# Kernel optimization log

Measured on AMD Instinct MI355X. Metric: run time of the kernel, lower is better.

The kernel has to match this reference:

```python
import jax, jax.numpy as jnp
import numpy as np
import math

B, C, H, W = 16, 512, 32, 32
NUM_HEADS = 8
EPS = 1e-5

def setup_inputs() -> dict:
    key = jax.random.key(0)
    ks = jax.random.split(key, 4)
    x = jax.random.normal(ks[0], (B, C, H, W), dtype=jnp.float32)
    emb = jax.random.normal(ks[1], (B, C), dtype=jnp.float32)
    w_qkv = jax.random.normal(ks[2], (3 * C, C), dtype=jnp.float32) * (1.0 / math.sqrt(C))
    b_qkv = jnp.zeros((3 * C,), dtype=jnp.float32)
    w_proj = jax.random.normal(ks[3], (C, C), dtype=jnp.float32) * (1.0 / math.sqrt(C))
    b_proj = jnp.zeros((C,), dtype=jnp.float32)
    return {"x": x, "emb": emb, "w_qkv": w_qkv, "b_qkv": b_qkv, "w_proj": w_proj, "b_proj": b_proj}


def reference(x, emb, w_qkv, b_qkv, w_proj, b_proj):
    b, c = x.shape[0], x.shape[1]
    spatial = x.shape[2:]
    xf = x.reshape(b, c, -1)                      # [b, c, T]
    # LayerNorm over channel dim (dim=1), no affine
    mu = jnp.mean(xf, axis=1, keepdims=True)
    var = jnp.var(xf, axis=1, keepdims=True)
    xn = (xf - mu) / jnp.sqrt(var + EPS)
    # 1x1 conv = channel GEMM: [3c,c] x [b,c,T] -> [b,3c,T]
    qkv = jnp.einsum('oc,bct->bot', w_qkv, xn) + b_qkv[None, :, None]
    T = qkv.shape[-1]
    qkv = qkv.reshape(b * NUM_HEADS, -1, T)       # [b*h, 3*hd, T]
    ch = qkv.shape[1] // 3
    q, k, v = jnp.split(qkv, 3, axis=1)
    scale = 1.0 / math.sqrt(math.sqrt(ch))
    w = jnp.einsum('bct,bcs->bts', q * scale, k * scale)  # [b*h, T, T]
    w = jax.nn.softmax(w.astype(jnp.float32), axis=-1).astype(qkv.dtype)
    h = jnp.einsum('bts,bcs->bct', w, v)          # [b*h, hd, T]
    h = h.reshape(b, -1, T)                        # [b, c, T]
    h = jnp.einsum('oc,bct->bot', w_proj, h) + b_proj[None, :, None]
    return (xf + h).reshape(b, c, *spatial)
```

## Files before the change

kernel.cpp:

```cpp
#include <hip/hip_runtime.h>


#define TSZ 1024
#define CCH 512
#define NBATCH 16

typedef __attribute__((ext_vector_type(8))) short short8;
typedef __attribute__((ext_vector_type(4))) float f32x4;
typedef __attribute__((ext_vector_type(4))) int i32x4;
typedef __attribute__((ext_vector_type(4))) unsigned u32x4;
typedef __attribute__((ext_vector_type(2))) unsigned u32x2;

__device__ inline short f2bf(float f) {
  unsigned u = __builtin_bit_cast(unsigned, f);
  u += 0x7fff + ((u >> 16) & 1);
  return (short)(u >> 16);
}

__device__ inline void gl16(const void* g, void* l) {
  __builtin_amdgcn_global_load_lds((const __attribute__((address_space(1))) void*)g,
                                   (__attribute__((address_space(3))) void*)l,
                                   16, 0, 0);
}

__global__ __launch_bounds__(256) void k_cvt(const float* __restrict__ wq,
                                             const float* __restrict__ wp,
                                             short* __restrict__ wqb,
                                             short* __restrict__ wpb) {
  int i = blockIdx.x * 256 + threadIdx.x;
  const int nq = 1536 * 512;
  if (i < nq) wqb[i] = f2bf(wq[i]);
  int j = i - nq;
  if (j >= 0 && j < 512 * 512) wpb[j] = f2bf(wp[j]);
}

__global__ __launch_bounds__(256) void k_ln(const float* __restrict__ x,
                                            short* __restrict__ xnT) {
  const int b = blockIdx.x;
  const int t0 = blockIdx.y * 64;
  const int tid = threadIdx.x;
  const int tt = tid & 63, cg = tid >> 6;

  __shared__ float red[2][4][64];
  __shared__ float mu_s[64], rs_s[64];
  __shared__ float xt[64][65];

  const float* xb = x + (long)b * CCH * TSZ;

  float s = 0.f, s2 = 0.f;
  for (int c = cg * 128; c < cg * 128 + 128; ++c) {
    float v = xb[(long)c * TSZ + t0 + tt];
    s += v; s2 += v * v;
  }
  red[0][cg][tt] = s; red[1][cg][tt] = s2;
  __syncthreads();
  if (tid < 64) {
    float ss = red[0][0][tid] + red[0][1][tid] + red[0][2][tid] + red[0][3][tid];
    float qq = red[1][0][tid] + red[1][1][tid] + red[1][2][tid] + red[1][3][tid];
    float mu = ss * (1.f / 512.f);
    float var = qq * (1.f / 512.f) - mu * mu;
    mu_s[tid] = mu;
    rs_s[tid] = rsqrtf(var + 1e-5f);
  }
  __syncthreads();

  for (int c0 = 0; c0 < CCH; c0 += 64) {
    for (int i = tid; i < 64 * 64; i += 256) {
      int ci = i >> 6, t2 = i & 63;
      xt[ci][t2] = xb[(long)(c0 + ci) * TSZ + t0 + t2];
    }
    __syncthreads();
    for (int i = tid; i < 64 * 64; i += 256) {
      int cc = i & 63, t2 = i >> 6;
      float v = (xt[cc][t2] - mu_s[t2]) * rs_s[t2];
      xnT[((long)b * TSZ + t0 + t2) * CCH + c0 + cc] = f2bf(v);
    }
    __syncthreads();
  }
}

__device__ inline int qkmap(int n) {
  if (n < 512) return (n >> 6) * 192 + (n & 63);
  int j = n - 512;
  return (j >> 6) * 192 + 64 + (j & 63);
}
__device__ inline int vmap(int m) {
  return (m >> 6) * 192 + 128 + (m & 63);
}

template <int MODE>
__global__ __launch_bounds__(256) void k_gemm(const short* __restrict__ Ab,
                                              const short* __restrict__ Bb,
                                              void* __restrict__ outb,
                                              const float* __restrict__ bias,
                                              const float* __restrict__ resid) {
  const int b = blockIdx.z;
  const int m0 = blockIdx.x * 128, n0 = blockIdx.y * 128;
  const int tid = threadIdx.x;
  const int lane = tid & 63, wv = tid >> 6;
  const int wm = wv >> 1, wn = wv & 1;
  const int l15 = lane & 15, lg = lane >> 4;

  const short* A = Ab + (MODE == 0 ? (long)b * TSZ * CCH : 0);
  const short* Bm = Bb + (MODE == 0 ? 0 : (long)b * TSZ * CCH);

  __shared__ __attribute__((aligned(16))) short sA[128 * 32];
  __shared__ __attribute__((aligned(16))) short sB[128 * 32];

  f32x4 acc[4][4];
#pragma unroll
  for (int i = 0; i < 4; ++i)
#pragma unroll
    for (int j = 0; j < 4; ++j) acc[i][j] = (f32x4){0.f, 0.f, 0.f, 0.f};

  long a_src[2], b_src[2];
#pragma unroll
  for (int q = 0; q < 2; ++q) {
    int idx = wv * 128 + q * 64 + lane;
    int row = idx >> 2, kc = (idx & 3) * 8;
    int am = m0 + row;
    int ar = (MODE == 1) ? vmap(am) : am;
    a_src[q] = (long)ar * CCH + kc;
    int bn = n0 + row;
    int br = (MODE == 0) ? qkmap(bn) : bn;
    b_src[q] = (long)br * CCH + kc;
  }

  for (int k0 = 0; k0 < CCH; k0 += 32) {
#pragma unroll
    for (int q = 0; q < 2; ++q) {
      gl16(A + a_src[q] + k0, sA + (wv * 128 + q * 64) * 8);
      gl16(Bm + b_src[q] + k0, sB + (wv * 128 + q * 64) * 8);
    }
    __syncthreads();
    short8 af[4], bfr[4];
#pragma unroll
    for (int i = 0; i < 4; ++i)
      af[i] = *(const short8*)(sA + ((wm * 64 + i * 16 + l15) * 32 + lg * 8));
#pragma unroll
    for (int j = 0; j < 4; ++j)
      bfr[j] = *(const short8*)(sB + ((wn * 64 + j * 16 + l15) * 32 + lg * 8));
#pragma unroll
    for (int i = 0; i < 4; ++i)
#pragma unroll
      for (int j = 0; j < 4; ++j)
        acc[i][j] = __builtin_amdgcn_mfma_f32_16x16x32_bf16(af[i], bfr[j], acc[i][j], 0, 0, 0);
    __syncthreads();
  }

#pragma unroll
  for (int i = 0; i < 4; ++i)
#pragma unroll
    for (int j = 0; j < 4; ++j)
#pragma unroll
      for (int r = 0; r < 4; ++r) {
        int mi = m0 + wm * 64 + i * 16 + lg * 4 + r;
        int ni = n0 + wn * 64 + j * 16 + l15;
        float val = acc[i][j][r];
        long o = (long)mi * TSZ + ni;
        if (MODE == 0) {
          val += bias[qkmap(ni)];
          if (ni < 512) val *= 0.18033688011112042f;
          ((short*)outb)[(long)b * TSZ * TSZ + o] = f2bf(val);
        } else if (MODE == 1) {
          val += bias[vmap(mi)];
          ((short*)outb)[(long)b * CCH * TSZ + o] = f2bf(val);
        } else {
          val += bias[mi] + resid[(long)b * CCH * TSZ + o];
          ((float*)outb)[(long)b * CCH * TSZ + o] = val;
        }
      }
}

__global__ __launch_bounds__(256, 4) void k_attn(const short* __restrict__ qk,
                                                 const short* __restrict__ vbuf,
                                                 short* __restrict__ hb) {
  const int wgid = blockIdx.y * gridDim.x + blockIdx.x;
  const int xcd = wgid & 7, kb = wgid >> 3;
  const int bh = xcd * 16 + (kb & 15);
  const int t0 = (kb >> 4) * 128;
  const int b = bh >> 3, h = bh & 7;
  const int tid = threadIdx.x;
  const int lane = tid & 63, w = tid >> 6;
  const int l15 = lane & 15, lg = lane >> 4;

  __shared__ __attribute__((aligned(16))) short kt[2][64 * 64];
  __shared__ __attribute__((aligned(16))) short vt[2][64 * 64];

  const short* qkb = qk + (long)b * TSZ * 1024;
  const short* vb = vbuf + (long)b * CCH * TSZ;

  short8 aq[2][2];
  {
    const short* qb = qkb + (long)(t0 + w * 32) * 1024 + h * 64;
#pragma unroll
    for (int jt = 0; jt < 2; ++jt)
#pragma unroll
      for (int kk = 0; kk < 2; ++kk)
        aq[jt][kk] = *(const short8*)(qb + (long)(jt * 16 + l15) * 1024 + kk * 32 + lg * 8);
  }

  f32x4 of[2][4];
  float lp[2] = {0.f, 0.f};
#pragma unroll
  for (int i = 0; i < 2; ++i)
#pragma unroll
    for (int nf = 0; nf < 4; ++nf) of[i][nf] = (f32x4){0.f, 0.f, 0.f, 0.f};

  int srow[2], scoff[2];
#pragma unroll
  for (int q = 0; q < 2; ++q) {
    int idx = w * 128 + q * 64 + lane;
    int row = idx >> 3;
    int byo = ((idx & 7) * 16) ^ ((row & 7) << 4);
    srow[q] = row;
    scoff[q] = byo >> 1;
  }

  long vsrc[2];
  int vdstA[2], vdstB[2];
#pragma unroll
  for (int q = 0; q < 2; ++q) {
    int idx = q * 256 + tid;
    int c = idx >> 3, s8 = (idx & 7) * 8;
    vsrc[q] = (long)(h * 64 + c) * TSZ + s8;
    int kk2 = s8 >> 5, h4 = (s8 >> 4) & 1, lgf0 = (s8 & 15) >> 2;
    int spA = kk2 * 32 + lgf0 * 8 + h4 * 4;
    vdstA[q] = ((c * 64 + spA) * 2) ^ ((c & 7) << 4);
    vdstB[q] = ((c * 64 + spA + 8) * 2) ^ ((c & 7) << 4);
  }

#define STAGE_K(buf, s0s)                                                      \
  {                                                                            \
    _Pragma("unroll") for (int q = 0; q < 2; ++q)                              \
      gl16(qkb + (long)((s0s) + srow[q]) * 1024 + 512 + h * 64 + scoff[q],     \
           kt[buf] + (w * 128 + q * 64) * 8);                                  \
  }

  u32x4 vreg0 = *(const u32x4*)(vb + vsrc[0]);
  u32x4 vreg1 = *(const u32x4*)(vb + vsrc[1]);
  STAGE_K(0, 0);
  *(u32x2*)((char*)vt[0] + vdstA[0]) = (u32x2){vreg0.x, vreg0.y};
  *(u32x2*)((char*)vt[0] + vdstB[0]) = (u32x2){vreg0.z, vreg0.w};
  *(u32x2*)((char*)vt[0] + vdstA[1]) = (u32x2){vreg1.x, vreg1.y};
  *(u32x2*)((char*)vt[0] + vdstB[1]) = (u32x2){vreg1.z, vreg1.w};
  __syncthreads();

  for (int s0 = 0; s0 < TSZ; s0 += 64) {
    const int cur = (s0 >> 6) & 1;
    const bool np = (s0 + 64 < TSZ);
    if (np) {
      vreg0 = *(const u32x4*)(vb + vsrc[0] + s0 + 64);
      vreg1 = *(const u32x4*)(vb + vsrc[1] + s0 + 64);
      STAGE_K(cur ^ 1, s0 + 64);
    }

    f32x4 sf[2][4];
#pragma unroll
    for (int jt = 0; jt < 2; ++jt)
#pragma unroll
      for (int ms = 0; ms < 4; ++ms) sf[jt][ms] = (f32x4){0.f, 0.f, 0.f, 0.f};
#pragma unroll
    for (int kk = 0; kk < 2; ++kk)
#pragma unroll
      for (int ms = 0; ms < 4; ++ms) {
        int srw = ms * 16 + l15;
        int byo = ((srw * 64 + kk * 32 + lg * 8) * 2) ^ ((srw & 7) << 4);
        short8 ka = *(const short8*)((const char*)kt[cur] + byo);
#pragma unroll
        for (int jt = 0; jt < 2; ++jt)
          sf[jt][ms] = __builtin_amdgcn_mfma_f32_16x16x32_bf16(ka, aq[jt][kk], sf[jt][ms], 0, 0, 0);
      }

    short8 apf[2][2];
#pragma unroll
    for (int jt = 0; jt < 2; ++jt) {
      float p[4][4];
#pragma unroll
      for (int ms = 0; ms < 4; ++ms)
#pragma unroll
        for (int r = 0; r < 4; ++r)
          p[ms][r] = exp2f(sf[jt][ms][r]);
#pragma unroll
      for (int ms = 0; ms < 4; ++ms)
        lp[jt] += (p[ms][0] + p[ms][1]) + (p[ms][2] + p[ms][3]);
      unsigned pk[4][2];
#pragma unroll
      for (int ms = 0; ms < 4; ++ms)
#pragma unroll
        for (int u = 0; u < 2; ++u)
          asm("v_cvt_pk_bf16_f32 %0, %1, %2" : "=v"(pk[ms][u])
              : "v"(p[ms][2 * u]), "v"(p[ms][2 * u + 1]));
#pragma unroll
      for (int kk = 0; kk < 2; ++kk) {
        i32x4 a32 = (i32x4){(int)pk[2 * kk][0], (int)pk[2 * kk][1],
                            (int)pk[2 * kk + 1][0], (int)pk[2 * kk + 1][1]};
        apf[jt][kk] = __builtin_bit_cast(short8, a32);
      }
    }

#pragma unroll
    for (int kk = 0; kk < 2; ++kk)
#pragma unroll
      for (int nf = 0; nf < 4; ++nf) {
        int cc = nf * 16 + l15;
        int byo = ((cc * 64 + kk * 32 + lg * 8) * 2) ^ ((cc & 7) << 4);
        short8 bv = *(const short8*)((const char*)vt[cur] + byo);
#pragma unroll
        for (int i = 0; i < 2; ++i)
          of[i][nf] = __builtin_amdgcn_mfma_f32_16x16x32_bf16(apf[i][kk], bv, of[i][nf], 0, 0, 0);
      }

    if (np) {
      *(u32x2*)((char*)vt[cur ^ 1] + vdstA[0]) = (u32x2){vreg0.x, vreg0.y};
      *(u32x2*)((char*)vt[cur ^ 1] + vdstB[0]) = (u32x2){vreg0.z, vreg0.w};
      *(u32x2*)((char*)vt[cur ^ 1] + vdstA[1]) = (u32x2){vreg1.x, vreg1.y};
      *(u32x2*)((char*)vt[cur ^ 1] + vdstB[1]) = (u32x2){vreg1.z, vreg1.w};
    }
    __syncthreads();
  }

  float linv[2][4];
#pragma unroll
  for (int i = 0; i < 2; ++i) {
    float ls = lp[i];
    ls += __shfl_xor(ls, 16);
    ls += __shfl_xor(ls, 32);
#pragma unroll
    for (int r = 0; r < 4; ++r)
      linv[i][r] = 1.0f / __shfl(ls, lg * 4 + r);
  }

#pragma unroll
  for (int i = 0; i < 2; ++i)
#pragma unroll
    for (int nf = 0; nf < 4; ++nf)
#pragma unroll
      for (int r = 0; r < 4; ++r) {
        int t = t0 + w * 32 + i * 16 + lg * 4 + r;
        int c = h * 64 + nf * 16 + l15;
        hb[((long)b * TSZ + t) * CCH + c] = f2bf(of[i][nf][r] * linv[i][r]);
      }
}

extern "C" void kernel_launch(void* const* d_in, const int* in_sizes, int n_in,
                              void* d_out, int out_size, void* d_ws, size_t ws_size,
                              hipStream_t stream) {
  const float* x = (const float*)d_in[0];
  const float* wq = (const float*)d_in[2];
  const float* bq = (const float*)d_in[3];
  const float* wp = (const float*)d_in[4];
  const float* bp = (const float*)d_in[5];

  char* ws = (char*)d_ws;
  short* wqb = (short*)ws;  ws += (long)1536 * 512 * 2;
  short* wpb = (short*)ws;  ws += (long)512 * 512 * 2;
  short* xnT = (short*)ws;  ws += (long)NBATCH * TSZ * CCH * 2;
  short* qkb = (short*)ws;  ws += (long)NBATCH * TSZ * 1024 * 2;
  short* vb  = (short*)ws;  ws += (long)NBATCH * CCH * TSZ * 2;
  short* hbuf = xnT;

  k_cvt<<<4096, 256, 0, stream>>>(wq, wp, wqb, wpb);
  k_ln<<<dim3(NBATCH, 16), 256, 0, stream>>>(x, xnT);
  k_gemm<0><<<dim3(8, 8, NBATCH), 256, 0, stream>>>(xnT, wqb, qkb, bq, nullptr);
  k_gemm<1><<<dim3(4, 8, NBATCH), 256, 0, stream>>>(wqb, xnT, vb, bq, nullptr);
  k_attn<<<dim3(8, 128), 256, 0, stream>>>(qkb, vb, hbuf);
  k_gemm<2><<<dim3(4, 8, NBATCH), 256, 0, stream>>>(wpb, hbuf, d_out, bp, x);
}
```

Measured before the change: 245.1 us.

## Double-buffer GEMM LDS staging, merge QK and V GEMMs, add XCD remap and setprio

```diff
diff --git a/kernel.cpp b/kernel.cpp
--- a/kernel.cpp
+++ b/kernel.cpp
@@ -88,24 +88,28 @@
   return (m >> 6) * 192 + 128 + (m & 63);
 }
 
-template <int MODE>
-__global__ __launch_bounds__(256) void k_gemm(const short* __restrict__ Ab,
-                                              const short* __restrict__ Bb,
-                                              void* __restrict__ outb,
-                                              const float* __restrict__ bias,
-                                              const float* __restrict__ resid) {
-  const int b = blockIdx.z;
-  const int m0 = blockIdx.x * 128, n0 = blockIdx.y * 128;
+__global__ __launch_bounds__(256) void k_qkv(const short* __restrict__ xnT,
+                                             const short* __restrict__ wqb,
+                                             short* __restrict__ qkb,
+                                             short* __restrict__ vbuf,
+                                             const float* __restrict__ bias) {
+  const int d = blockIdx.y * 96 + blockIdx.x;
+  const int orig = (d & 7) * 192 + (d >> 3);
+  const int z = orig / 96, wg = orig % 96;
+  const bool qkmode = wg < 64;
+  const int wgg = qkmode ? wg : wg - 64;
+  const int m0 = (wgg >> 3) * 128, n0 = (wgg & 7) * 128;
+
   const int tid = threadIdx.x;
   const int lane = tid & 63, wv = tid >> 6;
   const int wm = wv >> 1, wn = wv & 1;
   const int l15 = lane & 15, lg = lane >> 4;
 
-  const short* A = Ab + (MODE == 0 ? (long)b * TSZ * CCH : 0);
-  const short* Bm = Bb + (MODE == 0 ? 0 : (long)b * TSZ * CCH);
-
-  __shared__ __attribute__((aligned(16))) short sA[128 * 32];
-  __shared__ __attribute__((aligned(16))) short sB[128 * 32];
+  const short* A = qkmode ? xnT + (long)z * TSZ * CCH : wqb;
+  const short* Bm = qkmode ? wqb : xnT + (long)z * TSZ * CCH;
+
+  __shared__ __attribute__((aligned(16))) short sA[2][128 * 32];
+  __shared__ __attribute__((aligned(16))) short sB[2][128 * 32];
 
   f32x4 acc[4][4];
 #pragma unroll
@@ -118,33 +122,40 @@
   for (int q = 0; q < 2; ++q) {
     int idx = wv * 128 + q * 64 + lane;
     int row = idx >> 2, kc = (idx & 3) * 8;
-    int am = m0 + row;
-    int ar = (MODE == 1) ? vmap(am) : am;
+    int ar = qkmode ? (m0 + row) : vmap(m0 + row);
     a_src[q] = (long)ar * CCH + kc;
-    int bn = n0 + row;
-    int br = (MODE == 0) ? qkmap(bn) : bn;
+    int br = qkmode ? qkmap(n0 + row) : (n0 + row);
     b_src[q] = (long)br * CCH + kc;
   }
 
+#define GSTAGE(buf, k0s)                                                       \
+  {                                                                            \
+    _Pragma("unroll") for (int q = 0; q < 2; ++q) {                            \
+      gl16(A + a_src[q] + (k0s), sA[buf] + (wv * 128 + q * 64) * 8);           \
+      gl16(Bm + b_src[q] + (k0s), sB[buf] + (wv * 128 + q * 64) * 8);          \
+    }                                                                          \
+  }
+
+  GSTAGE(0, 0);
+  __syncthreads();
+
   for (int k0 = 0; k0 < CCH; k0 += 32) {
-#pragma unroll
-    for (int q = 0; q < 2; ++q) {
-      gl16(A + a_src[q] + k0, sA + (wv * 128 + q * 64) * 8);
-      gl16(Bm + b_src[q] + k0, sB + (wv * 128 + q * 64) * 8);
-    }
-    __syncthreads();
+    const int cur = (k0 >> 5) & 1;
+    if (k0 + 32 < CCH) GSTAGE(cur ^ 1, k0 + 32);
     short8 af[4], bfr[4];
 #pragma unroll
     for (int i = 0; i < 4; ++i)
-      af[i] = *(const short8*)(sA + ((wm * 64 + i * 16 + l15) * 32 + lg * 8));
+      af[i] = *(const short8*)(sA[cur] + ((wm * 64 + i * 16 + l15) * 32 + lg * 8));
 #pragma unroll
     for (int j = 0; j < 4; ++j)
-      bfr[j] = *(const short8*)(sB + ((wn * 64 + j * 16 + l15) * 32 + lg * 8));
+      bfr[j] = *(const short8*)(sB[cur] + ((wn * 64 + j * 16 + l15) * 32 + lg * 8));
+    __builtin_amdgcn_s_setprio(1);
 #pragma unroll
     for (int i = 0; i < 4; ++i)
 #pragma unroll
       for (int j = 0; j < 4; ++j)
         acc[i][j] = __builtin_amdgcn_mfma_f32_16x16x32_bf16(af[i], bfr[j], acc[i][j], 0, 0, 0);
+    __builtin_amdgcn_s_setprio(0);
     __syncthreads();
   }
 
@@ -158,17 +169,86 @@
         int ni = n0 + wn * 64 + j * 16 + l15;
         float val = acc[i][j][r];
         long o = (long)mi * TSZ + ni;
-        if (MODE == 0) {
+        if (qkmode) {
           val += bias[qkmap(ni)];
           if (ni < 512) val *= 0.18033688011112042f;
-          ((short*)outb)[(long)b * TSZ * TSZ + o] = f2bf(val);
-        } else if (MODE == 1) {
+          qkb[(long)z * TSZ * TSZ + o] = f2bf(val);
+        } else {
           val += bias[vmap(mi)];
-          ((short*)outb)[(long)b * CCH * TSZ + o] = f2bf(val);
-        } else {
-          val += bias[mi] + resid[(long)b * CCH * TSZ + o];
-          ((float*)outb)[(long)b * CCH * TSZ + o] = val;
+          vbuf[(long)z * CCH * TSZ + o] = f2bf(val);
         }
+      }
+}
+
+__global__ __launch_bounds__(256) void k_proj(const short* __restrict__ wpb,
+                                              const short* __restrict__ hbuf,
+                                              float* __restrict__ outp,
+                                              const float* __restrict__ bias,
+                                              const float* __restrict__ resid) {
+  const int d = blockIdx.y * 32 + blockIdx.x;
+  const int orig = (d & 7) * 64 + (d >> 3);
+  const int z = orig / 32, wg = orig % 32;
+  const int m0 = (wg >> 3) * 128, n0 = (wg & 7) * 128;
+
+  const int tid = threadIdx.x;
+  const int lane = tid & 63, wv = tid >> 6;
+  const int wm = wv >> 1, wn = wv & 1;
+  const int l15 = lane & 15, lg = lane >> 4;
+
+  const short* A = wpb;
+  const short* Bm = hbuf + (long)z * TSZ * CCH;
+
+  __shared__ __attribute__((aligned(16))) short sA[2][128 * 32];
+  __shared__ __attribute__((aligned(16))) short sB[2][128 * 32];
+
+  f32x4 acc[4][4];
+#pragma unroll
+  for (int i = 0; i < 4; ++i)
+#pragma unroll
+    for (int j = 0; j < 4; ++j) acc[i][j] = (f32x4){0.f, 0.f, 0.f, 0.f};
+
+  long a_src[2], b_src[2];
+#pragma unroll
+  for (int q = 0; q < 2; ++q) {
+    int idx = wv * 128 + q * 64 + lane;
+    int row = idx >> 2, kc = (idx & 3) * 8;
+    a_src[q] = (long)(m0 + row) * CCH + kc;
+    b_src[q] = (long)(n0 + row) * CCH + kc;
+  }
+
+  GSTAGE(0, 0);
+  __syncthreads();
+
+  for (int k0 = 0; k0 < CCH; k0 += 32) {
+    const int cur = (k0 >> 5) & 1;
+    if (k0 + 32 < CCH) GSTAGE(cur ^ 1, k0 + 32);
+    short8 af[4], bfr[4];
+#pragma unroll
+    for (int i = 0; i < 4; ++i)
+      af[i] = *(const short8*)(sA[cur] + ((wm * 64 + i * 16 + l15) * 32 + lg * 8));
+#pragma unroll
+    for (int j = 0; j < 4; ++j)
+      bfr[j] = *(const short8*)(sB[cur] + ((wn * 64 + j * 16 + l15) * 32 + lg * 8));
+    __builtin_amdgcn_s_setprio(1);
+#pragma unroll
+    for (int i = 0; i < 4; ++i)
+#pragma unroll
+      for (int j = 0; j < 4; ++j)
+        acc[i][j] = __builtin_amdgcn_mfma_f32_16x16x32_bf16(af[i], bfr[j], acc[i][j], 0, 0, 0);
+    __builtin_amdgcn_s_setprio(0);
+    __syncthreads();
+  }
+
+#pragma unroll
+  for (int i = 0; i < 4; ++i)
+#pragma unroll
+    for (int j = 0; j < 4; ++j)
+#pragma unroll
+      for (int r = 0; r < 4; ++r) {
+        int mi = m0 + wm * 64 + i * 16 + lg * 4 + r;
+        int ni = n0 + wn * 64 + j * 16 + l15;
+        long o = (long)z * CCH * TSZ + (long)mi * TSZ + ni;
+        outp[o] = acc[i][j][r] + bias[mi] + resid[o];
       }
 }
 
@@ -260,6 +340,7 @@
     for (int jt = 0; jt < 2; ++jt)
 #pragma unroll
       for (int ms = 0; ms < 4; ++ms) sf[jt][ms] = (f32x4){0.f, 0.f, 0.f, 0.f};
+    __builtin_amdgcn_s_setprio(1);
 #pragma unroll
     for (int kk = 0; kk < 2; ++kk)
 #pragma unroll
@@ -271,6 +352,7 @@
         for (int jt = 0; jt < 2; ++jt)
           sf[jt][ms] = __builtin_amdgcn_mfma_f32_16x16x32_bf16(ka, aq[jt][kk], sf[jt][ms], 0, 0, 0);
       }
+    __builtin_amdgcn_s_setprio(0);
 
     short8 apf[2][2];
 #pragma unroll
@@ -299,6 +381,7 @@
       }
     }
 
+    __builtin_amdgcn_s_setprio(1);
 #pragma unroll
     for (int kk = 0; kk < 2; ++kk)
 #pragma unroll
@@ -310,6 +393,7 @@
         for (int i = 0; i < 2; ++i)
           of[i][nf] = __builtin_amdgcn_mfma_f32_16x16x32_bf16(apf[i][kk], bv, of[i][nf], 0, 0, 0);
       }
+    __builtin_amdgcn_s_setprio(0);
 
     if (np) {
       *(u32x2*)((char*)vt[cur ^ 1] + vdstA[0]) = (u32x2){vreg0.x, vreg0.y};
@@ -362,8 +446,7 @@
 
   k_cvt<<<4096, 256, 0, stream>>>(wq, wp, wqb, wpb);
   k_ln<<<dim3(NBATCH, 16), 256, 0, stream>>>(x, xnT);
-  k_gemm<0><<<dim3(8, 8, NBATCH), 256, 0, stream>>>(xnT, wqb, qkb, bq, nullptr);
-  k_gemm<1><<<dim3(4, 8, NBATCH), 256, 0, stream>>>(wqb, xnT, vb, bq, nullptr);
+  k_qkv<<<dim3(96, 16), 256, 0, stream>>>(xnT, wqb, qkb, vb, bq);
   k_attn<<<dim3(8, 128), 256, 0, stream>>>(qkb, vb, hbuf);
-  k_gemm<2><<<dim3(4, 8, NBATCH), 256, 0, stream>>>(wpb, hbuf, d_out, bp, x);
-}
+  k_proj<<<dim3(32, 16), 256, 0, stream>>>(wpb, hbuf, (float*)d_out, bp, x);
+}
```

Result: slower. 273.9 us (+11.8%).
